# Kernel tuning notes

Hardware: AMD Instinct MI355X
Metric: run time of the kernel (lower is better)

Reference implementation:

```python
import jax, jax.numpy as jnp
import numpy as np

B, CIN, COUT, H, W = 16, 512, 128, 64, 64


def setup_inputs() -> dict:
    key = jax.random.key(0)
    k1, k2, k3 = jax.random.split(key, 3)
    x = jax.random.normal(k1, (B, CIN, H, W), dtype=jnp.float32)
    style = jax.random.normal(k2, (B, CIN), dtype=jnp.float32)
    # kaiming_normal_ on [COUT, CIN, 1, 1]: fan_in = CIN*1*1, std = sqrt(2/fan_in)
    weight = jax.random.normal(k3, (COUT, CIN), dtype=jnp.float32) * np.float32(np.sqrt(2.0 / CIN))
    return {"x": x, "style": style, "weight": weight}


def reference(x, style, weight):
    # Per-sample modulated weight: mw[b,o,c] = style[b,c] * weight[o,c]
    # 1x1 conv, padding=0, stride=1 -> batched channel-mixing GEMM:
    # out[b,o,h,w] = sum_c mw[b,o,c] * x[b,c,h,w]
    return jnp.einsum('oc,bc,bchw->bohw', weight, style, x)
```

## Files before the change

kernel.cpp:

```cpp
#include <hip/hip_runtime.h>
#include <stdint.h>

#define NB    16
#define CIN   512
#define COUT  128
#define HW    4096
#define NIT   16

using bf16x8  = __attribute__((ext_vector_type(8))) __bf16;
using floatx4 = __attribute__((ext_vector_type(4))) float;

__device__ __forceinline__ unsigned short f2bf_bits(float f) {
    union { float f; unsigned u; } v; v.f = f;
    return (unsigned short)((v.u + 0x7fffu + ((v.u >> 16) & 1u)) >> 16);
}

__global__ __launch_bounds__(256)
void modw_kernel(const float* __restrict__ style,
                 const float* __restrict__ weight,
                 __bf16* __restrict__ mw)
{
    const int id = blockIdx.x * 256 + threadIdx.x;
    const int k8 = id & 63;
    const int m  = (id >> 6) & 127;
    const int b  = id >> 13;

    const float4 w0 = *(const float4*)(weight + m * CIN + k8 * 8);
    const float4 w1 = *(const float4*)(weight + m * CIN + k8 * 8 + 4);
    const float4 s0 = *(const float4*)(style + b * CIN + k8 * 8);
    const float4 s1 = *(const float4*)(style + b * CIN + k8 * 8 + 4);

    union { unsigned short us[8]; bf16x8 v; } pk;
    pk.us[0] = f2bf_bits(w0.x * s0.x);
    pk.us[1] = f2bf_bits(w0.y * s0.y);
    pk.us[2] = f2bf_bits(w0.z * s0.z);
    pk.us[3] = f2bf_bits(w0.w * s0.w);
    pk.us[4] = f2bf_bits(w1.x * s1.x);
    pk.us[5] = f2bf_bits(w1.y * s1.y);
    pk.us[6] = f2bf_bits(w1.z * s1.z);
    pk.us[7] = f2bf_bits(w1.w * s1.w);
    *(bf16x8*)(mw + ((size_t)(b * 64 + k8) * 128 + m) * 8) = pk.v;
}

__global__ __launch_bounds__(256, 4)
void modconv1x1_kernel(const float* __restrict__ x,
                       const __bf16* __restrict__ mw,
                       float* __restrict__ out)
{
    const int tid  = threadIdx.x;
    const int lane = tid & 63;
    const int wave = tid >> 6;
    const int quad = lane >> 4;
    const int l15  = lane & 15;

    const int b     = blockIdx.x >> 6;
    const int idx   = (blockIdx.x & 63) * 4 + wave;
    const int mhalf = idx & 1;
    const int n0    = (idx >> 1) * 32;
    const int wm    = mhalf * 64;

    const float*  xb   = x   + (size_t)b * CIN * HW + n0;
    float*        outb = out + (size_t)b * COUT * HW + n0;
    const __bf16* mwb  = mw  + (size_t)b * (64 * 128 * 8);

    floatx4 acc[4][2];
    #pragma unroll
    for (int i = 0; i < 4; ++i)
        #pragma unroll
        for (int j = 0; j < 2; ++j)
            acc[i][j] = (floatx4){0.f, 0.f, 0.f, 0.f};

    bf16x8 afA[2][4];
    float  rbf[2][16];

#define LOAD_STAGE(S, ST)                                                      \
    {                                                                          \
        const __bf16* abase = mwb + (size_t)((4 * (S) + quad) * 128) * 8;      \
        _Pragma("unroll")                                                      \
        for (int tm = 0; tm < 4; ++tm)                                         \
            afA[ST][tm] = *(const bf16x8*)(abase + (wm + tm * 16 + l15) * 8);  \
        const float* src = xb + (size_t)((4 * (S) + quad) * 8) * HW + l15;     \
        _Pragma("unroll")                                                      \
        for (int tn = 0; tn < 2; ++tn)                                         \
            _Pragma("unroll")                                                  \
            for (int j = 0; j < 8; ++j)                                        \
                rbf[ST][tn * 8 + j] = src[(size_t)j * HW + tn * 16];           \
    }

    LOAD_STAGE(0, 0)

    for (int s = 0; s < NIT; ++s) {
        const int cur = s & 1;
        if (s + 1 < NIT) LOAD_STAGE(s + 1, cur ^ 1)

        bf16x8 bfr[2];
        #pragma unroll
        for (int tn = 0; tn < 2; ++tn) {
            union { unsigned short us[8]; bf16x8 v; } pk;
            #pragma unroll
            for (int j = 0; j < 8; ++j)
                pk.us[j] = f2bf_bits(rbf[cur][tn * 8 + j]);
            bfr[tn] = pk.v;
        }
        #pragma unroll
        for (int tm = 0; tm < 4; ++tm)
            #pragma unroll
            for (int tn = 0; tn < 2; ++tn)
                acc[tm][tn] = __builtin_amdgcn_mfma_f32_16x16x32_bf16(
                    afA[cur][tm], bfr[tn], acc[tm][tn], 0, 0, 0);
    }
#undef LOAD_STAGE

    #pragma unroll
    for (int tm = 0; tm < 4; ++tm) {
        const int o = wm + tm * 16 + quad * 4;
        #pragma unroll
        for (int tn = 0; tn < 2; ++tn) {
            const int n = tn * 16 + l15;
            #pragma unroll
            for (int r = 0; r < 4; ++r)
                outb[(size_t)(o + r) * HW + n] = acc[tm][tn][r];
        }
    }
}

extern "C" void kernel_launch(void* const* d_in, const int* in_sizes, int n_in,
                              void* d_out, int out_size, void* d_ws, size_t ws_size,
                              hipStream_t stream) {
    const float* x      = (const float*)d_in[0];
    const float* style  = (const float*)d_in[1];
    const float* weight = (const float*)d_in[2];
    float* out = (float*)d_out;
    __bf16* mw = (__bf16*)d_ws;

    modw_kernel<<<dim3(512), dim3(256), 0, stream>>>(style, weight, mw);
    modconv1x1_kernel<<<dim3(NB * 64), dim3(256), 0, stream>>>(x, mw, out);
}
```

Before: 218.8 us.

## Stage A and X tiles through LDS with global_load_lds double buffering

Rewrites the GEMM main loop so each block cooperatively copies the modulated-weight tile and a 32x64 x tile into LDS using direct global-to-LDS loads, double buffered with a barrier per iteration. Waves then read their fragments from LDS, and the block tile becomes 128x64 with waves split 2x2. Before this, each wave loaded its own registers straight from global memory. The change is meant to cut redundant global traffic and make loads wider and coalesced. It adds LDS usage and a sync each iteration, and the fp32 reads from LDS may hit bank conflicts.

```diff
diff --git a/kernel.cpp b/kernel.cpp
--- a/kernel.cpp
+++ b/kernel.cpp
@@ -5,7 +5,9 @@
 #define CIN   512
 #define COUT  128
 #define HW    4096
-#define NIT   16
+#define BN    64
+#define BK    32
+#define NIT   (CIN / BK)
 
 using bf16x8  = __attribute__((ext_vector_type(8))) __bf16;
 using floatx4 = __attribute__((ext_vector_type(4))) float;
@@ -14,6 +16,11 @@
     union { float f; unsigned u; } v; v.f = f;
     return (unsigned short)((v.u + 0x7fffu + ((v.u >> 16) & 1u)) >> 16);
 }
+
+#define GLD16(g, l)                                                            \
+    __builtin_amdgcn_global_load_lds(                                          \
+        (const __attribute__((address_space(1))) void*)(g),                    \
+        (__attribute__((address_space(3))) void*)(l), 16, 0, 0)
 
 __global__ __launch_bounds__(256)
 void modw_kernel(const float* __restrict__ style,
@@ -47,21 +54,27 @@
                        const __bf16* __restrict__ mw,
                        float* __restrict__ out)
 {
+    __shared__ __align__(16) __bf16 Alds[2][4096];
+    __shared__ __align__(16) float  Blds[2][BK * BN];
+
     const int tid  = threadIdx.x;
     const int lane = tid & 63;
     const int wave = tid >> 6;
     const int quad = lane >> 4;
     const int l15  = lane & 15;
 
-    const int b     = blockIdx.x >> 6;
-    const int idx   = (blockIdx.x & 63) * 4 + wave;
-    const int mhalf = idx & 1;
-    const int n0    = (idx >> 1) * 32;
-    const int wm    = mhalf * 64;
+    const int b  = blockIdx.x >> 6;
+    const int n0 = (blockIdx.x & 63) * BN;
 
-    const float*  xb   = x   + (size_t)b * CIN * HW + n0;
-    float*        outb = out + (size_t)b * COUT * HW + n0;
-    const __bf16* mwb  = mw  + (size_t)b * (64 * 128 * 8);
+    const char*  xbb  = (const char*)(x + (size_t)b * CIN * HW + n0);
+    float*       outb = out + (size_t)b * COUT * HW + n0;
+    const char*  mwb  = (const char*)mw + (size_t)b * (64 * 128 * 16);
+
+    const int wm = (wave & 1) * 64;
+    const int wn = (wave >> 1) * 32;
+
+    const int brow = lane >> 4;
+    const int bcol = lane & 15;
 
     floatx4 acc[4][2];
     #pragma unroll
@@ -70,28 +83,33 @@
         for (int j = 0; j < 2; ++j)
             acc[i][j] = (floatx4){0.f, 0.f, 0.f, 0.f};
 
-    bf16x8 afA[2][4];
-    float  rbf[2][16];
-
-#define LOAD_STAGE(S, ST)                                                      \
+#define STAGE(K0, BUF)                                                         \
     {                                                                          \
-        const __bf16* abase = mwb + (size_t)((4 * (S) + quad) * 128) * 8;      \
+        const char* at = mwb + (size_t)(K0) * 256;                             \
+        char*       al = (char*)&Alds[BUF][0];                                 \
+        GLD16(at + wave * 2048 + lane * 16,        al + wave * 2048);          \
+        GLD16(at + wave * 2048 + 1024 + lane * 16, al + wave * 2048 + 1024);   \
+        char* bl = (char*)&Blds[BUF][0];                                       \
         _Pragma("unroll")                                                      \
-        for (int tm = 0; tm < 4; ++tm)                                         \
-            afA[ST][tm] = *(const bf16x8*)(abase + (wm + tm * 16 + l15) * 8);  \
-        const float* src = xb + (size_t)((4 * (S) + quad) * 8) * HW + l15;     \
-        _Pragma("unroll")                                                      \
-        for (int tn = 0; tn < 2; ++tn)                                         \
-            _Pragma("unroll")                                                  \
-            for (int j = 0; j < 8; ++j)                                        \
-                rbf[ST][tn * 8 + j] = src[(size_t)j * HW + tn * 16];           \
+        for (int g = 0; g < 2; ++g) {                                          \
+            const int r = wave * 8 + g * 4 + brow;                             \
+            GLD16(xbb + (size_t)((K0) + r) * (HW * 4) + bcol * 16,             \
+                  bl + (wave * 8 + g * 4) * 256);                              \
+        }                                                                      \
     }
 
-    LOAD_STAGE(0, 0)
+    STAGE(0, 0)
 
-    for (int s = 0; s < NIT; ++s) {
-        const int cur = s & 1;
-        if (s + 1 < NIT) LOAD_STAGE(s + 1, cur ^ 1)
+    int cur = 0;
+    for (int it = 0; it < NIT; ++it) {
+        __syncthreads();
+
+        if (it + 1 < NIT) STAGE((it + 1) * BK, cur ^ 1)
+
+        bf16x8 af[4];
+        #pragma unroll
+        for (int tm = 0; tm < 4; ++tm)
+            af[tm] = *(const bf16x8*)&Alds[cur][(quad * COUT + wm + tm * 16 + l15) * 8];
 
         bf16x8 bfr[2];
         #pragma unroll
@@ -99,24 +117,27 @@
             union { unsigned short us[8]; bf16x8 v; } pk;
             #pragma unroll
             for (int j = 0; j < 8; ++j)
-                pk.us[j] = f2bf_bits(rbf[cur][tn * 8 + j]);
+                pk.us[j] = f2bf_bits(Blds[cur][(quad * 8 + j) * BN + wn + tn * 16 + l15]);
             bfr[tn] = pk.v;
         }
+
         #pragma unroll
         for (int tm = 0; tm < 4; ++tm)
             #pragma unroll
             for (int tn = 0; tn < 2; ++tn)
                 acc[tm][tn] = __builtin_amdgcn_mfma_f32_16x16x32_bf16(
-                    afA[cur][tm], bfr[tn], acc[tm][tn], 0, 0, 0);
+                    af[tm], bfr[tn], acc[tm][tn], 0, 0, 0);
+
+        cur ^= 1;
     }
-#undef LOAD_STAGE
+#undef STAGE
 
     #pragma unroll
     for (int tm = 0; tm < 4; ++tm) {
         const int o = wm + tm * 16 + quad * 4;
         #pragma unroll
         for (int tn = 0; tn < 2; ++tn) {
-            const int n = tn * 16 + l15;
+            const int n = wn + tn * 16 + l15;
             #pragma unroll
             for (int r = 0; r < 4; ++r)
                 outb[(size_t)(o + r) * HW + n] = acc[tm][tn][r];
```

Result: faster. 210.9 us (-3.6%).
